# Performance work log

Measured on AMD Instinct MI355X. Metric: run time of the kernel, lower is better.

## Reference

```python
import jax, jax.numpy as jnp
import numpy as np

N = 50000      # nodes
E = 500000     # edges (avg degree 10)
IN = 256       # in_feats
HID = 64       # hid_feats (per-head out dim)
H = 4          # num_heads


def setup_inputs() -> dict:
    key = jax.random.key(0)
    ks = jax.random.split(key, 16)
    f32 = jnp.float32
    def rn(k, shape, s=0.05):
        return jax.random.normal(k, shape, dtype=f32) * s
    return {
        "x": jax.random.normal(ks[0], (N, IN), dtype=f32),
        "src": jax.random.randint(ks[1], (E,), 0, N, dtype=jnp.int32),
        "dst": jax.random.randint(ks[2], (E,), 0, N, dtype=jnp.int32),
        "embed_W": rn(ks[3], (IN, HID)), "embed_b": jnp.zeros((HID,), f32),
        "W1": rn(ks[4], (HID, H * HID)),
        "al1": rn(ks[5], (H, HID)), "ar1": rn(ks[6], (H, HID)),
        "b1": jnp.zeros((H * HID,), f32),
        "W2": rn(ks[7], (H * HID, H * HID)),
        "al2": rn(ks[8], (H, HID)), "ar2": rn(ks[9], (H, HID)),
        "b2": jnp.zeros((H * HID,), f32),
        "p1_W": rn(ks[10], (H * HID, HID)), "p1_b": jnp.zeros((HID,), f32),
        "p2_W": rn(ks[11], (HID, 1)), "p2_b": jnp.zeros((1,), f32),
    }


def _gat_conv(x, W, al, ar, b, src, dst):
    """DGL GATConv: linear proj, per-edge LeakyReLU attention, edge softmax over dst, scatter-sum."""
    feat = (x @ W).reshape(N, H, HID)                    # [N,H,F]
    el = jnp.einsum('nhf,hf->nh', feat, al)              # [N,H]
    er = jnp.einsum('nhf,hf->nh', feat, ar)              # [N,H]
    e = jax.nn.leaky_relu(el[src] + er[dst], 0.2)        # [E,H]
    m = jax.ops.segment_max(e, dst, num_segments=N)      # per-dst max (stable softmax)
    ex = jnp.exp(e - m[dst])                             # [E,H]
    s = jax.ops.segment_sum(ex, dst, num_segments=N)     # [N,H]
    alpha = ex / s[dst]                                  # edge softmax weights
    out = jax.ops.segment_sum(alpha[:, :, None] * feat[src], dst, num_segments=N)  # [N,H,F]
    return out + b.reshape(1, H, HID)


def reference(x, src, dst, embed_W, embed_b, W1, al1, ar1, b1,
              W2, al2, ar2, b2, p1_W, p1_b, p2_W, p2_b):
    h = x @ embed_W + embed_b                                        # embed: [N,HID]
    h = jax.nn.relu(_gat_conv(h, W1, al1, ar1, b1, src, dst))        # [N,H,HID]
    h = h.reshape(N, H * HID)
    h = jax.nn.relu(_gat_conv(h, W2, al2, ar2, b2, src, dst))        # [N,H,HID]
    h = h.reshape(N, H * HID)
    return jax.nn.sigmoid((h @ p1_W + p1_b) @ p2_W + p2_b)           # [N,1]
```

## Files before the change

### kernel.cpp

```cpp
#include <hip/hip_runtime.h>
#include <hip/hip_bf16.h>

#define NN 50000
#define NE 500000
#define C_HH 256

typedef __attribute__((ext_vector_type(8))) short s16x8;
typedef __attribute__((ext_vector_type(4))) float f32x4;
typedef __attribute__((ext_vector_type(4))) unsigned short u16x4;
typedef unsigned short ushort_t;

__device__ __forceinline__ float lrelu(float x) { return x > 0.f ? x : 0.2f * x; }

__device__ __forceinline__ ushort_t f2bf(float f) {
  unsigned u = __float_as_uint(f);
  u = (u + 0x7FFFu + ((u >> 16) & 1u)) >> 16;
  return (ushort_t)u;
}
__device__ __forceinline__ float bf2f(ushort_t u) {
  return __uint_as_float(((unsigned)u) << 16);
}
__device__ __forceinline__ float sel_head(float4 v, int head) {
  const float x0 = (head & 1) ? v.y : v.x;
  const float x1 = (head & 1) ? v.w : v.z;
  return (head & 2) ? x1 : x0;
}

__global__ __launch_bounds__(256) void prep_kernel(const float* __restrict__ eW,
                                                   const float* __restrict__ W1,
                                                   const float* __restrict__ W2,
                                                   const float* __restrict__ p1W,
                                                   ushort_t* __restrict__ eWT,
                                                   ushort_t* __restrict__ w1T,
                                                   ushort_t* __restrict__ w2T,
                                                   ushort_t* __restrict__ p1T) {
  int idx = blockIdx.x * 256 + threadIdx.x;
  if (idx < 16384) {
    eWT[idx] = f2bf(eW[(idx & 255) * 64 + (idx >> 8)]);
  } else if (idx < 32768) {
    idx -= 16384;
    w1T[idx] = f2bf(W1[(idx & 63) * 256 + (idx >> 6)]);
  } else if (idx < 98304) {
    idx -= 32768;
    w2T[idx] = f2bf(W2[(idx & 255) * 256 + (idx >> 8)]);
  } else if (idx < 114688) {
    idx -= 98304;
    p1T[idx] = f2bf(p1W[(idx & 255) * 64 + (idx >> 8)]);
  }
}

template <int K, int NC, bool A_F32, bool BIAS, int EPI>
__global__ __launch_bounds__(256) void gemm_mfma(const void* __restrict__ Ain,
                                                 const ushort_t* __restrict__ WT,
                                                 const float* __restrict__ Bias,
                                                 void* __restrict__ Cout, int M,
                                                 const float* __restrict__ al,
                                                 const float* __restrict__ ar,
                                                 float* __restrict__ el,
                                                 float* __restrict__ er,
                                                 const float* __restrict__ p2w,
                                                 const float* __restrict__ p2b,
                                                 float* __restrict__ out) {
  constexpr int NT = NC / 16;
  constexpr int KS = K / 32;
  const int wid = threadIdx.x >> 6;
  const int lane = threadIdx.x & 63;
  const int row0 = blockIdx.x * 128 + wid * 32;
  const int rA = lane & 15;
  const int kg = lane >> 4;

  f32x4 acc[2][NT] = {};
  const s16x8 zf = {0, 0, 0, 0, 0, 0, 0, 0};

  const bool v0 = (row0 + rA) < M;
  const bool v1 = (row0 + 16 + rA) < M;
  const ushort_t* Wrow = WT + rA * K;

  if (A_F32) {
    const float* Af = (const float*)Ain;
    const float* Arow0 = Af + (size_t)(row0 + rA) * K;
    const float* Arow1 = Af + (size_t)(row0 + 16 + rA) * K;
    for (int ks = 0; ks < KS; ++ks) {
      const int k0 = ks * 32 + kg * 8;
      s16x8 a0 = zf, a1 = zf;
      if (v0) {
        const f32x4 u0 = *reinterpret_cast<const f32x4*>(Arow0 + k0);
        const f32x4 u1 = *reinterpret_cast<const f32x4*>(Arow0 + k0 + 4);
        a0[0] = (short)f2bf(u0[0]); a0[1] = (short)f2bf(u0[1]);
        a0[2] = (short)f2bf(u0[2]); a0[3] = (short)f2bf(u0[3]);
        a0[4] = (short)f2bf(u1[0]); a0[5] = (short)f2bf(u1[1]);
        a0[6] = (short)f2bf(u1[2]); a0[7] = (short)f2bf(u1[3]);
      }
      if (v1) {
        const f32x4 u0 = *reinterpret_cast<const f32x4*>(Arow1 + k0);
        const f32x4 u1 = *reinterpret_cast<const f32x4*>(Arow1 + k0 + 4);
        a1[0] = (short)f2bf(u0[0]); a1[1] = (short)f2bf(u0[1]);
        a1[2] = (short)f2bf(u0[2]); a1[3] = (short)f2bf(u0[3]);
        a1[4] = (short)f2bf(u1[0]); a1[5] = (short)f2bf(u1[1]);
        a1[6] = (short)f2bf(u1[2]); a1[7] = (short)f2bf(u1[3]);
      }
#pragma unroll
      for (int nt = 0; nt < NT; ++nt) {
        const s16x8 b = *reinterpret_cast<const s16x8*>(Wrow + nt * 16 * K + k0);
        acc[0][nt] = __builtin_amdgcn_mfma_f32_16x16x32_bf16(a0, b, acc[0][nt], 0, 0, 0);
        acc[1][nt] = __builtin_amdgcn_mfma_f32_16x16x32_bf16(a1, b, acc[1][nt], 0, 0, 0);
      }
    }
  } else {
    const ushort_t* Ab = (const ushort_t*)Ain;
    const ushort_t* Arow0 = Ab + (size_t)(row0 + rA) * K;
    const ushort_t* Arow1 = Ab + (size_t)(row0 + 16 + rA) * K;
    for (int ks = 0; ks < KS; ++ks) {
      const int k0 = ks * 32 + kg * 8;
      const s16x8 a0 = v0 ? *reinterpret_cast<const s16x8*>(Arow0 + k0) : zf;
      const s16x8 a1 = v1 ? *reinterpret_cast<const s16x8*>(Arow1 + k0) : zf;
#pragma unroll
      for (int nt = 0; nt < NT; ++nt) {
        const s16x8 b = *reinterpret_cast<const s16x8*>(Wrow + nt * 16 * K + k0);
        acc[0][nt] = __builtin_amdgcn_mfma_f32_16x16x32_bf16(a0, b, acc[0][nt], 0, 0, 0);
        acc[1][nt] = __builtin_amdgcn_mfma_f32_16x16x32_bf16(a1, b, acc[1][nt], 0, 0, 0);
      }
    }
  }

  if (EPI <= 2) {
#pragma unroll
    for (int nt = 0; nt < NT; ++nt) {
      const int col = nt * 16 + rA;
      const float bv = BIAS ? Bias[col] : 0.f;
#pragma unroll
      for (int mt = 0; mt < 2; ++mt) {
#pragma unroll
        for (int i = 0; i < 4; ++i) {
          const int row = row0 + mt * 16 + kg * 4 + i;
          if (row < M) {
            const float v = acc[mt][nt][i] + bv;
            if (EPI == 0)
              reinterpret_cast<float*>(Cout)[(size_t)row * NC + col] = v;
            else
              reinterpret_cast<ushort_t*>(Cout)[(size_t)row * NC + col] = f2bf(v);
          }
        }
      }
    }
  }

  if (EPI == 2) {
    float alv[NT], arv[NT];
#pragma unroll
    for (int nt = 0; nt < NT; ++nt) {
      alv[nt] = al[nt * 16 + rA];
      arv[nt] = ar[nt * 16 + rA];
    }
#pragma unroll
    for (int mt = 0; mt < 2; ++mt) {
#pragma unroll
      for (int i = 0; i < 4; ++i) {
        float e0 = 0.f, e1 = 0.f, e2 = 0.f, e3 = 0.f;
        float r0 = 0.f, r1 = 0.f, r2 = 0.f, r3 = 0.f;
#pragma unroll
        for (int j = 0; j < 4; ++j) {
          e0 = fmaf(acc[mt][0 + j][i], alv[0 + j], e0);
          e1 = fmaf(acc[mt][4 + j][i], alv[4 + j], e1);
          e2 = fmaf(acc[mt][8 + j][i], alv[8 + j], e2);
          e3 = fmaf(acc[mt][12 + j][i], alv[12 + j], e3);
          r0 = fmaf(acc[mt][0 + j][i], arv[0 + j], r0);
          r1 = fmaf(acc[mt][4 + j][i], arv[4 + j], r1);
          r2 = fmaf(acc[mt][8 + j][i], arv[8 + j], r2);
          r3 = fmaf(acc[mt][12 + j][i], arv[12 + j], r3);
        }
#pragma unroll
        for (int m = 1; m < 16; m <<= 1) {
          e0 += __shfl_xor(e0, m); e1 += __shfl_xor(e1, m);
          e2 += __shfl_xor(e2, m); e3 += __shfl_xor(e3, m);
          r0 += __shfl_xor(r0, m); r1 += __shfl_xor(r1, m);
          r2 += __shfl_xor(r2, m); r3 += __shfl_xor(r3, m);
        }
        const int row = row0 + mt * 16 + kg * 4 + i;
        if (rA == 0 && row < M) {
          *reinterpret_cast<float4*>(el + row * 4) = make_float4(e0, e1, e2, e3);
          *reinterpret_cast<float4*>(er + row * 4) = make_float4(r0, r1, r2, r3);
        }
      }
    }
  }

  if (EPI == 3) {
    float pv[NT], bb[NT];
#pragma unroll
    for (int nt = 0; nt < NT; ++nt) {
      pv[nt] = p2w[nt * 16 + rA];
      bb[nt] = BIAS ? Bias[nt * 16 + rA] : 0.f;
    }
    const float p2bias = p2b[0];
#pragma unroll
    for (int mt = 0; mt < 2; ++mt) {
#pragma unroll
      for (int i = 0; i < 4; ++i) {
        float v = 0.f;
#pragma unroll
        for (int nt = 0; nt < NT; ++nt) v = fmaf(acc[mt][nt][i] + bb[nt], pv[nt], v);
#pragma unroll
        for (int m = 1; m < 16; m <<= 1) v += __shfl_xor(v, m);
        const int row = row0 + mt * 16 + kg * 4 + i;
        if (rA == 0 && row < M) out[row] = 1.f / (1.f + __expf(-(v + p2bias)));
      }
    }
  }
}

__global__ __launch_bounds__(256) void hist_kernel(const int* __restrict__ dst,
                                                   int* __restrict__ rowptr) {
  const int e = blockIdx.x * 256 + threadIdx.x;
  if (e < NE) atomicAdd(&rowptr[dst[e]], 1);
}

__global__ __launch_bounds__(256) void scan1_kernel(int* __restrict__ rowptr,
                                                    int* __restrict__ partial) {
  __shared__ int sh[256];
  const int t = threadIdx.x;
  const int i = blockIdx.x * 256 + t;
  const int v = (i < NN) ? rowptr[i] : 0;
  sh[t] = v;
  __syncthreads();
#pragma unroll
  for (int off = 1; off < 256; off <<= 1) {
    int x = (t >= off) ? sh[t - off] : 0;
    __syncthreads();
    sh[t] += x;
    __syncthreads();
  }
  if (i < NN) rowptr[i] = sh[t] - v;
  if (t == 255) partial[blockIdx.x] = sh[255];
}

__global__ __launch_bounds__(256) void scan2_kernel(int* __restrict__ partial, int npb) {
  __shared__ int sh[256];
  const int t = threadIdx.x;
  const int v = (t < npb) ? partial[t] : 0;
  sh[t] = v;
  __syncthreads();
#pragma unroll
  for (int off = 1; off < 256; off <<= 1) {
    int x = (t >= off) ? sh[t - off] : 0;
    __syncthreads();
    sh[t] += x;
    __syncthreads();
  }
  if (t < npb) partial[t] = sh[t] - v;
}

__global__ __launch_bounds__(256) void scan3_kernel(int* __restrict__ rowptr,
                                                    const int* __restrict__ partial,
                                                    int* __restrict__ cursor) {
  const int i = blockIdx.x * 256 + threadIdx.x;
  if (i < NN) {
    const int r = rowptr[i] + partial[i >> 8];
    rowptr[i] = r;
    cursor[i] = r;
  } else if (i == NN) {
    rowptr[NN] = NE;
  }
}

__global__ __launch_bounds__(256) void scatter_kernel(const int* __restrict__ src,
                                                      const int* __restrict__ dst,
                                                      int* __restrict__ cursor,
                                                      int* __restrict__ sorted_src) {
  const int e = blockIdx.x * 256 + threadIdx.x;
  if (e >= NE) return;
  const int pos = atomicAdd(&cursor[dst[e]], 1);
  sorted_src[pos] = src[e];
}

__global__ __launch_bounds__(256) void aggr_fused_kernel(const int* __restrict__ rowptr,
                                                         const int* __restrict__ sorted_src,
                                                         const float* __restrict__ el,
                                                         const float* __restrict__ er,
                                                         const ushort_t* __restrict__ featb,
                                                         const float* __restrict__ bias,
                                                         ushort_t* __restrict__ out) {
  const int node = blockIdx.x * 4 + (threadIdx.x >> 6);
  const int lane = threadIdx.x & 63;
  const int head = lane >> 4;
  const int start = rowptr[node];
  const int end = rowptr[node + 1];
  const float erh = sel_head(*reinterpret_cast<const float4*>(er + node * 4), head);
  const size_t lofs = (size_t)lane * 4;

  float a0 = 0.f, a1 = 0.f, a2 = 0.f, a3 = 0.f, s = 0.f;
  int e = start;
  const int end4 = end - 3;
  for (; e < end4; e += 4) {
    const int sn0 = sorted_src[e + 0];
    const int sn1 = sorted_src[e + 1];
    const int sn2 = sorted_src[e + 2];
    const int sn3 = sorted_src[e + 3];
    const float4 A0 = *reinterpret_cast<const float4*>(el + sn0 * 4);
    const float4 A1 = *reinterpret_cast<const float4*>(el + sn1 * 4);
    const float4 A2 = *reinterpret_cast<const float4*>(el + sn2 * 4);
    const float4 A3 = *reinterpret_cast<const float4*>(el + sn3 * 4);
    const u16x4 F0 = *reinterpret_cast<const u16x4*>(featb + (size_t)sn0 * C_HH + lofs);
    const u16x4 F1 = *reinterpret_cast<const u16x4*>(featb + (size_t)sn1 * C_HH + lofs);
    const u16x4 F2 = *reinterpret_cast<const u16x4*>(featb + (size_t)sn2 * C_HH + lofs);
    const u16x4 F3 = *reinterpret_cast<const u16x4*>(featb + (size_t)sn3 * C_HH + lofs);
    const float w0 = __expf(lrelu(sel_head(A0, head) + erh));
    const float w1 = __expf(lrelu(sel_head(A1, head) + erh));
    const float w2 = __expf(lrelu(sel_head(A2, head) + erh));
    const float w3 = __expf(lrelu(sel_head(A3, head) + erh));
    a0 = fmaf(w0, bf2f(F0[0]), a0); a1 = fmaf(w0, bf2f(F0[1]), a1);
    a2 = fmaf(w0, bf2f(F0[2]), a2); a3 = fmaf(w0, bf2f(F0[3]), a3);
    a0 = fmaf(w1, bf2f(F1[0]), a0); a1 = fmaf(w1, bf2f(F1[1]), a1);
    a2 = fmaf(w1, bf2f(F1[2]), a2); a3 = fmaf(w1, bf2f(F1[3]), a3);
    a0 = fmaf(w2, bf2f(F2[0]), a0); a1 = fmaf(w2, bf2f(F2[1]), a1);
    a2 = fmaf(w2, bf2f(F2[2]), a2); a3 = fmaf(w2, bf2f(F2[3]), a3);
    a0 = fmaf(w3, bf2f(F3[0]), a0); a1 = fmaf(w3, bf2f(F3[1]), a1);
    a2 = fmaf(w3, bf2f(F3[2]), a2); a3 = fmaf(w3, bf2f(F3[3]), a3);
    s += (w0 + w1) + (w2 + w3);
  }
  for (; e < end; ++e) {
    const int sn = sorted_src[e];
    const float4 A = *reinterpret_cast<const float4*>(el + sn * 4);
    const u16x4 F = *reinterpret_cast<const u16x4*>(featb + (size_t)sn * C_HH + lofs);
    const float w = __expf(lrelu(sel_head(A, head) + erh));
    a0 = fmaf(w, bf2f(F[0]), a0); a1 = fmaf(w, bf2f(F[1]), a1);
    a2 = fmaf(w, bf2f(F[2]), a2); a3 = fmaf(w, bf2f(F[3]), a3);
    s += w;
  }

  float r0 = 0.f, r1 = 0.f, r2 = 0.f, r3 = 0.f;
  if (end > start) {
    const float inv = 1.f / s;
    r0 = a0 * inv; r1 = a1 * inv; r2 = a2 * inv; r3 = a3 * inv;
  }
  const float4 bb = *reinterpret_cast<const float4*>(bias + lane * 4);
  u16x4 o;
  o[0] = f2bf(fmaxf(r0 + bb.x, 0.f));
  o[1] = f2bf(fmaxf(r1 + bb.y, 0.f));
  o[2] = f2bf(fmaxf(r2 + bb.z, 0.f));
  o[3] = f2bf(fmaxf(r3 + bb.w, 0.f));
  *reinterpret_cast<u16x4*>(out + (size_t)node * C_HH + lane * 4) = o;
}

extern "C" void kernel_launch(void* const* d_in, const int* in_sizes, int n_in,
                              void* d_out, int out_size, void* d_ws, size_t ws_size,
                              hipStream_t stream) {
  const float* x = (const float*)d_in[0];
  const int* src = (const int*)d_in[1];
  const int* dst = (const int*)d_in[2];
  const float* embed_W = (const float*)d_in[3];
  const float* embed_b = (const float*)d_in[4];
  const float* W1 = (const float*)d_in[5];
  const float* al1 = (const float*)d_in[6];
  const float* ar1 = (const float*)d_in[7];
  const float* b1 = (const float*)d_in[8];
  const float* W2 = (const float*)d_in[9];
  const float* al2 = (const float*)d_in[10];
  const float* ar2 = (const float*)d_in[11];
  const float* b2 = (const float*)d_in[12];
  const float* p1_W = (const float*)d_in[13];
  const float* p1_b = (const float*)d_in[14];
  const float* p2_W = (const float*)d_in[15];
  const float* p2_b = (const float*)d_in[16];

  char* ws = (char*)d_ws;
  ushort_t* featb = (ushort_t*)(ws + 0);
  ushort_t* houtb = (ushort_t*)(ws + 25600000);
  ushort_t* h0b = (ushort_t*)(ws + 51200000);
  float* el = (float*)(ws + 57600000);
  float* er = (float*)(ws + 58400000);
  int* rowptr = (int*)(ws + 59200000);
  int* cursor = (int*)(ws + 59500000);
  int* partial = (int*)(ws + 59800000);
  int* sorted_src = (int*)(ws + 59900000);
  ushort_t* eWT = (ushort_t*)(ws + 62000000);
  ushort_t* w1T = (ushort_t*)(ws + 62100000);
  ushort_t* w2T = (ushort_t*)(ws + 62200000);
  ushort_t* p1T = (ushort_t*)(ws + 62400000);

  const int gEdge = (NE + 255) / 256;
  const int nScanB = (NN + 255) / 256;
  const int gGemm = (NN + 127) / 128;
  const int gNode = NN / 4;

  hipMemsetAsync(rowptr, 0, (NN + 1) * sizeof(int), stream);
  hist_kernel<<<gEdge, 256, 0, stream>>>(dst, rowptr);
  scan1_kernel<<<nScanB, 256, 0, stream>>>(rowptr, partial);
  scan2_kernel<<<1, 256, 0, stream>>>(partial, nScanB);
  scan3_kernel<<<nScanB + 1, 256, 0, stream>>>(rowptr, partial, cursor);
  scatter_kernel<<<gEdge, 256, 0, stream>>>(src, dst, cursor, sorted_src);

  prep_kernel<<<448, 256, 0, stream>>>(embed_W, W1, W2, p1_W, eWT, w1T, w2T, p1T);

  gemm_mfma<256, 64, true, true, 1><<<gGemm, 256, 0, stream>>>(
      x, eWT, embed_b, h0b, NN, nullptr, nullptr, nullptr, nullptr, nullptr, nullptr, nullptr);

  gemm_mfma<64, 256, false, false, 2><<<gGemm, 256, 0, stream>>>(
      h0b, w1T, nullptr, featb, NN, al1, ar1, el, er, nullptr, nullptr, nullptr);
  aggr_fused_kernel<<<gNode, 256, 0, stream>>>(rowptr, sorted_src, el, er, featb, b1, houtb);

  gemm_mfma<256, 256, false, false, 2><<<gGemm, 256, 0, stream>>>(
      houtb, w2T, nullptr, featb, NN, al2, ar2, el, er, nullptr, nullptr, nullptr);
  aggr_fused_kernel<<<gNode, 256, 0, stream>>>(rowptr, sorted_src, el, er, featb, b2, houtb);

  gemm_mfma<256, 64, false, true, 3><<<gGemm, 256, 0, stream>>>(
      houtb, p1T, p1_b, nullptr, NN, nullptr, nullptr, nullptr, nullptr, p2_W, p2_b, (float*)d_out);
}
```

Measured before the change: 406.5 us.

## Fold embed into W1 and collapse prediction head into a vector dot

Precomputes embed_W@W1 (and embed_b@W1) so the embedding GEMM and the first GAT projection become a single 256x256 GEMM directly on x, removing the h0 intermediate. It also folds p1_W@p2_W into one 256-vector plus a scalar, replacing the final GEMM with a per-node dot-product kernel. The GEMM is retiled so each wave computes 64 columns (one head) for 32 rows. The cost is a larger first GEMM (K=256, N=256 instead of 256x64 then 64x256) and a different bf16 rounding path, since intermediates are no longer rounded to bf16.

After: 379.2 us. -6.7%, faster.

```diff
diff --git a/kernel.cpp b/kernel.cpp
--- a/kernel.cpp
+++ b/kernel.cpp
@@ -28,182 +28,152 @@
 
 __global__ __launch_bounds__(256) void prep_kernel(const float* __restrict__ eW,
                                                    const float* __restrict__ W1,
+                                                   const float* __restrict__ eb,
                                                    const float* __restrict__ W2,
                                                    const float* __restrict__ p1W,
-                                                   ushort_t* __restrict__ eWT,
-                                                   ushort_t* __restrict__ w1T,
+                                                   const float* __restrict__ p1b,
+                                                   const float* __restrict__ p2W,
+                                                   const float* __restrict__ p2b,
+                                                   ushort_t* __restrict__ WcT,
                                                    ushort_t* __restrict__ w2T,
-                                                   ushort_t* __restrict__ p1T) {
+                                                   float* __restrict__ bc,
+                                                   float* __restrict__ qv,
+                                                   float* __restrict__ cv) {
   int idx = blockIdx.x * 256 + threadIdx.x;
-  if (idx < 16384) {
-    eWT[idx] = f2bf(eW[(idx & 255) * 64 + (idx >> 8)]);
-  } else if (idx < 32768) {
-    idx -= 16384;
-    w1T[idx] = f2bf(W1[(idx & 63) * 256 + (idx >> 6)]);
-  } else if (idx < 98304) {
-    idx -= 32768;
-    w2T[idx] = f2bf(W2[(idx & 255) * 256 + (idx >> 8)]);
-  } else if (idx < 114688) {
-    idx -= 98304;
-    p1T[idx] = f2bf(p1W[(idx & 255) * 64 + (idx >> 8)]);
-  }
-}
-
-template <int K, int NC, bool A_F32, bool BIAS, int EPI>
-__global__ __launch_bounds__(256) void gemm_mfma(const void* __restrict__ Ain,
-                                                 const ushort_t* __restrict__ WT,
-                                                 const float* __restrict__ Bias,
-                                                 void* __restrict__ Cout, int M,
-                                                 const float* __restrict__ al,
-                                                 const float* __restrict__ ar,
-                                                 float* __restrict__ el,
-                                                 float* __restrict__ er,
-                                                 const float* __restrict__ p2w,
-                                                 const float* __restrict__ p2b,
-                                                 float* __restrict__ out) {
-  constexpr int NT = NC / 16;
-  constexpr int KS = K / 32;
+  if (idx < 65536) {
+    const int n = idx >> 8, k = idx & 255;
+    float s = 0.f;
+#pragma unroll 8
+    for (int j = 0; j < 64; ++j) s = fmaf(eW[k * 64 + j], W1[j * 256 + n], s);
+    WcT[idx] = f2bf(s);
+  } else if (idx < 131072) {
+    idx -= 65536;
+    const int n = idx >> 8, k = idx & 255;
+    w2T[idx] = f2bf(W2[k * 256 + n]);
+  } else if (idx < 131328) {
+    const int n = idx - 131072;
+    float s = 0.f;
+#pragma unroll 8
+    for (int j = 0; j < 64; ++j) s = fmaf(eb[j], W1[j * 256 + n], s);
+    bc[n] = s;
+  } else if (idx < 131584) {
+    const int k = idx - 131328;
+    float s = 0.f;
+#pragma unroll 8
+    for (int j = 0; j < 64; ++j) s = fmaf(p1W[k * 64 + j], p2W[j], s);
+    qv[k] = s;
+  } else if (idx == 131584) {
+    float s = p2b[0];
+    for (int j = 0; j < 64; ++j) s = fmaf(p1b[j], p2W[j], s);
+    cv[0] = s;
+  }
+}
+
+template <bool A_F32, bool BIAS>
+__global__ __launch_bounds__(256) void gemm_fused(const void* __restrict__ Ain,
+                                                  const ushort_t* __restrict__ WT,
+                                                  const float* __restrict__ bc,
+                                                  const float* __restrict__ al,
+                                                  const float* __restrict__ ar,
+                                                  float* __restrict__ el,
+                                                  float* __restrict__ er,
+                                                  ushort_t* __restrict__ Cout, int M) {
   const int wid = threadIdx.x >> 6;
   const int lane = threadIdx.x & 63;
-  const int row0 = blockIdx.x * 128 + wid * 32;
+  const int row0 = blockIdx.x * 32;
   const int rA = lane & 15;
   const int kg = lane >> 4;
-
-  f32x4 acc[2][NT] = {};
+  const int c0 = wid * 64;
+
+  f32x4 acc[2][4] = {};
   const s16x8 zf = {0, 0, 0, 0, 0, 0, 0, 0};
-
   const bool v0 = (row0 + rA) < M;
   const bool v1 = (row0 + 16 + rA) < M;
-  const ushort_t* Wrow = WT + rA * K;
-
-  if (A_F32) {
-    const float* Af = (const float*)Ain;
-    const float* Arow0 = Af + (size_t)(row0 + rA) * K;
-    const float* Arow1 = Af + (size_t)(row0 + 16 + rA) * K;
-    for (int ks = 0; ks < KS; ++ks) {
-      const int k0 = ks * 32 + kg * 8;
-      s16x8 a0 = zf, a1 = zf;
+  const ushort_t* Wbase = WT + (size_t)(c0 + rA) * 256;
+
+  for (int ks = 0; ks < 8; ++ks) {
+    const int k0 = ks * 32 + kg * 8;
+    s16x8 a0 = zf, a1 = zf;
+    if (A_F32) {
+      const float* Af = (const float*)Ain;
       if (v0) {
-        const f32x4 u0 = *reinterpret_cast<const f32x4*>(Arow0 + k0);
-        const f32x4 u1 = *reinterpret_cast<const f32x4*>(Arow0 + k0 + 4);
+        const f32x4 u0 = *reinterpret_cast<const f32x4*>(Af + (size_t)(row0 + rA) * 256 + k0);
+        const f32x4 u1 = *reinterpret_cast<const f32x4*>(Af + (size_t)(row0 + rA) * 256 + k0 + 4);
         a0[0] = (short)f2bf(u0[0]); a0[1] = (short)f2bf(u0[1]);
         a0[2] = (short)f2bf(u0[2]); a0[3] = (short)f2bf(u0[3]);
         a0[4] = (short)f2bf(u1[0]); a0[5] = (short)f2bf(u1[1]);
         a0[6] = (short)f2bf(u1[2]); a0[7] = (short)f2bf(u1[3]);
       }
       if (v1) {
-        const f32x4 u0 = *reinterpret_cast<const f32x4*>(Arow1 + k0);
-        const f32x4 u1 = *reinterpret_cast<const f32x4*>(Arow1 + k0 + 4);
+        const f32x4 u0 = *reinterpret_cast<const f32x4*>(Af + (size_t)(row0 + 16 + rA) * 256 + k0);
+        const f32x4 u1 = *reinterpret_cast<const f32x4*>(Af + (size_t)(row0 + 16 + rA) * 256 + k0 + 4);
         a1[0] = (short)f2bf(u0[0]); a1[1] = (short)f2bf(u0[1]);
         a1[2] = (short)f2bf(u0[2]); a1[3] = (short)f2bf(u0[3]);
         a1[4] = (short)f2bf(u1[0]); a1[5] = (short)f2bf(u1[1]);
         a1[6] = (short)f2bf(u1[2]); a1[7] = (short)f2bf(u1[3]);
       }
-#pragma unroll
-      for (int nt = 0; nt < NT; ++nt) {
-        const s16x8 b = *reinterpret_cast<const s16x8*>(Wrow + nt * 16 * K + k0);
-        acc[0][nt] = __builtin_amdgcn_mfma_f32_16x16x32_bf16(a0, b, acc[0][nt], 0, 0, 0);
-        acc[1][nt] = __builtin_amdgcn_mfma_f32_16x16x32_bf16(a1, b, acc[1][nt], 0, 0, 0);
-      }
-    }
-  } else {
-    const ushort_t* Ab = (const ushort_t*)Ain;
-    const ushort_t* Arow0 = Ab + (size_t)(row0 + rA) * K;
-    const ushort_t* Arow1 = Ab + (size_t)(row0 + 16 + rA) * K;
-    for (int ks = 0; ks < KS; ++ks) {
-      const int k0 = ks * 32 + kg * 8;
-      const s16x8 a0 = v0 ? *reinterpret_cast<const s16x8*>(Arow0 + k0) : zf;
-      const s16x8 a1 = v1 ? *reinterpret_cast<const s16x8*>(Arow1 + k0) : zf;
-#pragma unroll
-      for (int nt = 0; nt < NT; ++nt) {
-        const s16x8 b = *reinterpret_cast<const s16x8*>(Wrow + nt * 16 * K + k0);
-        acc[0][nt] = __builtin_amdgcn_mfma_f32_16x16x32_bf16(a0, b, acc[0][nt], 0, 0, 0);
-        acc[1][nt] = __builtin_amdgcn_mfma_f32_16x16x32_bf16(a1, b, acc[1][nt], 0, 0, 0);
-      }
-    }
-  }
-
-  if (EPI <= 2) {
-#pragma unroll
-    for (int nt = 0; nt < NT; ++nt) {
-      const int col = nt * 16 + rA;
-      const float bv = BIAS ? Bias[col] : 0.f;
-#pragma unroll
-      for (int mt = 0; mt < 2; ++mt) {
-#pragma unroll
-        for (int i = 0; i < 4; ++i) {
-          const int row = row0 + mt * 16 + kg * 4 + i;
-          if (row < M) {
-            const float v = acc[mt][nt][i] + bv;
-            if (EPI == 0)
-              reinterpret_cast<float*>(Cout)[(size_t)row * NC + col] = v;
-            else
-              reinterpret_cast<ushort_t*>(Cout)[(size_t)row * NC + col] = f2bf(v);
-          }
-        }
-      }
-    }
-  }
-
-  if (EPI == 2) {
-    float alv[NT], arv[NT];
-#pragma unroll
-    for (int nt = 0; nt < NT; ++nt) {
-      alv[nt] = al[nt * 16 + rA];
-      arv[nt] = ar[nt * 16 + rA];
-    }
+    } else {
+      const ushort_t* Ab = (const ushort_t*)Ain;
+      if (v0) a0 = *reinterpret_cast<const s16x8*>(Ab + (size_t)(row0 + rA) * 256 + k0);
+      if (v1) a1 = *reinterpret_cast<const s16x8*>(Ab + (size_t)(row0 + 16 + rA) * 256 + k0);
+    }
+#pragma unroll
+    for (int nt = 0; nt < 4; ++nt) {
+      const s16x8 b = *reinterpret_cast<const s16x8*>(Wbase + nt * 16 * 256 + k0);
+      acc[0][nt] = __builtin_amdgcn_mfma_f32_16x16x32_bf16(a0, b, acc[0][nt], 0, 0, 0);
+      acc[1][nt] = __builtin_amdgcn_mfma_f32_16x16x32_bf16(a1, b, acc[1][nt], 0, 0, 0);
+    }
+  }
+
+  if (BIAS) {
+#pragma unroll
+    for (int nt = 0; nt < 4; ++nt) {
+      const float bv = bc[c0 + nt * 16 + rA];
+#pragma unroll
+      for (int mt = 0; mt < 2; ++mt)
+#pragma unroll
+        for (int i = 0; i < 4; ++i) acc[mt][nt][i] += bv;
+    }
+  }
+
+#pragma unroll
+  for (int nt = 0; nt < 4; ++nt) {
+    const int col = c0 + nt * 16 + rA;
 #pragma unroll
     for (int mt = 0; mt < 2; ++mt) {
 #pragma unroll
       for (int i = 0; i < 4; ++i) {
-        float e0 = 0.f, e1 = 0.f, e2 = 0.f, e3 = 0.f;
-        float r0 = 0.f, r1 = 0.f, r2 = 0.f, r3 = 0.f;
-#pragma unroll
-        for (int j = 0; j < 4; ++j) {
-          e0 = fmaf(acc[mt][0 + j][i], alv[0 + j], e0);
-          e1 = fmaf(acc[mt][4 + j][i], alv[4 + j], e1);
-          e2 = fmaf(acc[mt][8 + j][i], alv[8 + j], e2);
-          e3 = fmaf(acc[mt][12 + j][i], alv[12 + j], e3);
-          r0 = fmaf(acc[mt][0 + j][i], arv[0 + j], r0);
-          r1 = fmaf(acc[mt][4 + j][i], arv[4 + j], r1);
-          r2 = fmaf(acc[mt][8 + j][i], arv[8 + j], r2);
-          r3 = fmaf(acc[mt][12 + j][i], arv[12 + j], r3);
-        }
-#pragma unroll
-        for (int m = 1; m < 16; m <<= 1) {
-          e0 += __shfl_xor(e0, m); e1 += __shfl_xor(e1, m);
-          e2 += __shfl_xor(e2, m); e3 += __shfl_xor(e3, m);
-          r0 += __shfl_xor(r0, m); r1 += __shfl_xor(r1, m);
-          r2 += __shfl_xor(r2, m); r3 += __shfl_xor(r3, m);
-        }
         const int row = row0 + mt * 16 + kg * 4 + i;
-        if (rA == 0 && row < M) {
-          *reinterpret_cast<float4*>(el + row * 4) = make_float4(e0, e1, e2, e3);
-          *reinterpret_cast<float4*>(er + row * 4) = make_float4(r0, r1, r2, r3);
-        }
-      }
-    }
-  }
-
-  if (EPI == 3) {
-    float pv[NT], bb[NT];
-#pragma unroll
-    for (int nt = 0; nt < NT; ++nt) {
-      pv[nt] = p2w[nt * 16 + rA];
-      bb[nt] = BIAS ? Bias[nt * 16 + rA] : 0.f;
-    }
-    const float p2bias = p2b[0];
-#pragma unroll
-    for (int mt = 0; mt < 2; ++mt) {
-#pragma unroll
-      for (int i = 0; i < 4; ++i) {
-        float v = 0.f;
-#pragma unroll
-        for (int nt = 0; nt < NT; ++nt) v = fmaf(acc[mt][nt][i] + bb[nt], pv[nt], v);
-#pragma unroll
-        for (int m = 1; m < 16; m <<= 1) v += __shfl_xor(v, m);
-        const int row = row0 + mt * 16 + kg * 4 + i;
-        if (rA == 0 && row < M) out[row] = 1.f / (1.f + __expf(-(v + p2bias)));
+        if (row < M) Cout[(size_t)row * 256 + col] = f2bf(acc[mt][nt][i]);
+      }
+    }
+  }
+
+  float alv[4], arv[4];
+#pragma unroll
+  for (int nt = 0; nt < 4; ++nt) {
+    alv[nt] = al[c0 + nt * 16 + rA];
+    arv[nt] = ar[c0 + nt * 16 + rA];
+  }
+#pragma unroll
+  for (int mt = 0; mt < 2; ++mt) {
+#pragma unroll
+    for (int i = 0; i < 4; ++i) {
+      float e = 0.f, r = 0.f;
+#pragma unroll
+      for (int nt = 0; nt < 4; ++nt) {
+        e = fmaf(acc[mt][nt][i], alv[nt], e);
+        r = fmaf(acc[mt][nt][i], arv[nt], r);
+      }
+#pragma unroll
+      for (int m = 1; m < 16; m <<= 1) {
+        e += __shfl_xor(e, m);
+        r += __shfl_xor(r, m);
+      }
+      const int row = row0 + mt * 16 + kg * 4 + i;
+      if (rA == 0 && row < M) {
+        el[row * 4 + wid] = e;
+        er[row * 4 + wid] = r;
       }
     }
   }
@@ -342,6 +312,20 @@
   *reinterpret_cast<u16x4*>(out + (size_t)node * C_HH + lane * 4) = o;
 }
 
+__global__ __launch_bounds__(256) void head_kernel(const ushort_t* __restrict__ houtb,
+                                                   const float* __restrict__ qv,
+                                                   const float* __restrict__ cv,
+                                                   float* __restrict__ out) {
+  const int node = blockIdx.x * 4 + (threadIdx.x >> 6);
+  const int lane = threadIdx.x & 63;
+  const u16x4 f = *reinterpret_cast<const u16x4*>(houtb + (size_t)node * C_HH + lane * 4);
+  const float4 q = *reinterpret_cast<const float4*>(qv + lane * 4);
+  float v = bf2f(f[0]) * q.x + bf2f(f[1]) * q.y + bf2f(f[2]) * q.z + bf2f(f[3]) * q.w;
+#pragma unroll
+  for (int off = 32; off; off >>= 1) v += __shfl_xor(v, off);
+  if (lane == 0) out[node] = 1.f / (1.f + __expf(-(v + cv[0])));
+}
+
 extern "C" void kernel_launch(void* const* d_in, const int* in_sizes, int n_in,
                               void* d_out, int out_size, void* d_ws, size_t ws_size,
                               hipStream_t stream) {
@@ -366,21 +350,21 @@
   char* ws = (char*)d_ws;
   ushort_t* featb = (ushort_t*)(ws + 0);
   ushort_t* houtb = (ushort_t*)(ws + 25600000);
-  ushort_t* h0b = (ushort_t*)(ws + 51200000);
-  float* el = (float*)(ws + 57600000);
-  float* er = (float*)(ws + 58400000);
-  int* rowptr = (int*)(ws + 59200000);
-  int* cursor = (int*)(ws + 59500000);
-  int* partial = (int*)(ws + 59800000);
-  int* sorted_src = (int*)(ws + 59900000);
-  ushort_t* eWT = (ushort_t*)(ws + 62000000);
-  ushort_t* w1T = (ushort_t*)(ws + 62100000);
-  ushort_t* w2T = (ushort_t*)(ws + 62200000);
-  ushort_t* p1T = (ushort_t*)(ws + 62400000);
+  float* el = (float*)(ws + 51200000);
+  float* er = (float*)(ws + 52000000);
+  int* rowptr = (int*)(ws + 52800000);
+  int* cursor = (int*)(ws + 53100000);
+  int* partial = (int*)(ws + 53400000);
+  int* sorted_src = (int*)(ws + 53500000);
+  ushort_t* WcT = (ushort_t*)(ws + 55600000);
+  ushort_t* w2T = (ushort_t*)(ws + 55800000);
+  float* bc = (float*)(ws + 56000000);
+  float* qv = (float*)(ws + 56010000);
+  float* cv = (float*)(ws + 56020000);
 
   const int gEdge = (NE + 255) / 256;
   const int nScanB = (NN + 255) / 256;
-  const int gGemm = (NN + 127) / 128;
+  const int gGemm = (NN + 31) / 32;
   const int gNode = NN / 4;
 
   hipMemsetAsync(rowptr, 0, (NN + 1) * sizeof(int), stream);
@@ -390,19 +374,14 @@
   scan3_kernel<<<nScanB + 1, 256, 0, stream>>>(rowptr, partial, cursor);
   scatter_kernel<<<gEdge, 256, 0, stream>>>(src, dst, cursor, sorted_src);
 
-  prep_kernel<<<448, 256, 0, stream>>>(embed_W, W1, W2, p1_W, eWT, w1T, w2T, p1T);
-
-  gemm_mfma<256, 64, true, true, 1><<<gGemm, 256, 0, stream>>>(
-      x, eWT, embed_b, h0b, NN, nullptr, nullptr, nullptr, nullptr, nullptr, nullptr, nullptr);
-
-  gemm_mfma<64, 256, false, false, 2><<<gGemm, 256, 0, stream>>>(
-      h0b, w1T, nullptr, featb, NN, al1, ar1, el, er, nullptr, nullptr, nullptr);
+  prep_kernel<<<515, 256, 0, stream>>>(embed_W, W1, embed_b, W2, p1_W, p1_b, p2_W, p2_b,
+                                       WcT, w2T, bc, qv, cv);
+
+  gemm_fused<true, true><<<gGemm, 256, 0, stream>>>(x, WcT, bc, al1, ar1, el, er, featb, NN);
   aggr_fused_kernel<<<gNode, 256, 0, stream>>>(rowptr, sorted_src, el, er, featb, b1, houtb);
 
-  gemm_mfma<256, 256, false, false, 2><<<gGemm, 256, 0, stream>>>(
-      houtb, w2T, nullptr, featb, NN, al2, ar2, el, er, nullptr, nullptr, nullptr);
+  gemm_fused<false, false><<<gGemm, 256, 0, stream>>>(houtb, w2T, nullptr, al2, ar2, el, er, featb, NN);
   aggr_fused_kernel<<<gNode, 256, 0, stream>>>(rowptr, sorted_src, el, er, featb, b2, houtb);
 
-  gemm_mfma<256, 64, false, true, 3><<<gGemm, 256, 0, stream>>>(
-      houtb, p1T, p1_b, nullptr, NN, nullptr, nullptr, nullptr, nullptr, p2_W, p2_b, (float*)d_out);
-}
+  head_kernel<<<gNode, 256, 0, stream>>>(houtb, qv, cv, (float*)d_out);
+}
```
